# Kernel optimization log

Hardware: AMD Instinct MI355X
Metric: run time of the kernel (lower is better)

The kernel has to match this reference:

```python
import jax, jax.numpy as jnp
import numpy as np

N_NODES = 50000
N_EDGES = 800000
NEG_SLOPE = 0.2  # leaky_relu slope used in the model


def setup_inputs() -> dict:
    key = jax.random.key(0)
    ks = jax.random.split(key, 8)
    d_in, d_h, d_out = 64, 64, 4
    x = jax.random.normal(ks[0], (N_NODES, d_in), dtype=jnp.float32)
    edge_index = jax.random.randint(ks[1], (2, N_EDGES), 0, N_NODES, dtype=jnp.int32)
    # Glorot-style init like PyG GCNConv
    W0 = jax.random.normal(ks[2], (d_in, d_h), dtype=jnp.float32) * np.float32(1.0 / np.sqrt(d_in))
    W1 = jax.random.normal(ks[3], (d_h, d_h), dtype=jnp.float32) * np.float32(1.0 / np.sqrt(d_h))
    W2 = jax.random.normal(ks[4], (d_h, d_out), dtype=jnp.float32) * np.float32(1.0 / np.sqrt(d_h))
    b0 = jnp.zeros((d_h,), dtype=jnp.float32)
    b1 = jnp.zeros((d_h,), dtype=jnp.float32)
    b2 = jnp.zeros((d_out,), dtype=jnp.float32)
    return {"x": x, "edge_index": edge_index, "W0": W0, "b0": b0,
            "W1": W1, "b1": b1, "W2": W2, "b2": b2}


def _gcn_norm(edge_index, n_nodes, dtype):
    # Add self-loops, compute symmetric normalization D^{-1/2} (A+I) D^{-1/2}
    src, dst = edge_index[0], edge_index[1]
    loop = jnp.arange(n_nodes, dtype=src.dtype)
    src = jnp.concatenate([src, loop])
    dst = jnp.concatenate([dst, loop])
    deg = jax.ops.segment_sum(jnp.ones_like(dst, dtype=dtype), dst, num_segments=n_nodes)
    dinv = jnp.where(deg > 0, jax.lax.rsqrt(deg), jnp.zeros_like(deg))
    norm = dinv[src] * dinv[dst]  # [E + N]
    return src, dst, norm


def _gcn_layer(h, src, dst, norm, W, b, n_nodes):
    h = h @ W                                  # [N, d_out]
    msg = h[src] * norm[:, None]               # gather + edge scaling
    out = jax.ops.segment_sum(msg, dst, num_segments=n_nodes)  # scatter-add
    return out + b


def reference(x, edge_index, W0, b0, W1, b1, W2, b2):
    # Eval-mode forward: dropout_edge and F.dropout are identity when not training.
    n = x.shape[0]
    src, dst, norm = _gcn_norm(edge_index, n, x.dtype)
    h = _gcn_layer(x, src, dst, norm, W0, b0, n)
    h = jax.nn.leaky_relu(h, NEG_SLOPE)
    h = _gcn_layer(h, src, dst, norm, W1, b1, n)
    h = jax.nn.leaky_relu(h, NEG_SLOPE)
    out = _gcn_layer(h, src, dst, norm, W2, b2, n)
    return out
```

## Files before the change

### kernel.cpp

```cpp
#include <hip/hip_runtime.h>
#include <math.h>

#define NEG_SLOPE 0.2f
#define NPAD 50176
#define NW8  (NPAD / 4)
#define NCHUNK 256

__global__ __launch_bounds__(1024) void k_hist(const int* __restrict__ dst,
                                               unsigned int* __restrict__ histw,
                                               unsigned char* __restrict__ rank,
                                               int e, int es) {
    extern __shared__ unsigned int lcnt[];
    int t = threadIdx.x;
    for (int w = t; w < NW8; w += 1024) lcnt[w] = 0u;
    __syncthreads();
    int beg = blockIdx.x * es;
    int end = min(beg + es, e);
    for (int i = beg + t; i < end; i += 1024) {
        int d = dst[i];
        int sh = (d & 3) << 3;
        unsigned int old = atomicAdd(&lcnt[d >> 2], 1u << sh);
        rank[i] = (unsigned char)((old >> sh) & 0xffu);
    }
    __syncthreads();
    unsigned int* out = histw + (size_t)blockIdx.x * NW8;
    for (int w = t; w < NW8; w += 1024) out[w] = lcnt[w];
}

__global__ __launch_bounds__(256) void k_chscan(unsigned char* __restrict__ hist8,
                                                float* __restrict__ dinv,
                                                unsigned short* __restrict__ deg16,
                                                int* __restrict__ bsum, int n) {
    int t = threadIdx.x;
    int i = blockIdx.x * 256 + t;
    unsigned char* p = hist8 + i;
    unsigned int run = 0;
    for (int c = 0; c < NCHUNK; c += 8) {
        size_t b = (size_t)c * NPAD;
        unsigned char v0 = p[b];
        unsigned char v1 = p[b + (size_t)1 * NPAD];
        unsigned char v2 = p[b + (size_t)2 * NPAD];
        unsigned char v3 = p[b + (size_t)3 * NPAD];
        unsigned char v4 = p[b + (size_t)4 * NPAD];
        unsigned char v5 = p[b + (size_t)5 * NPAD];
        unsigned char v6 = p[b + (size_t)6 * NPAD];
        unsigned char v7 = p[b + (size_t)7 * NPAD];
        unsigned int e0 = run;
        unsigned int e1 = e0 + v0;
        unsigned int e2 = e1 + v1;
        unsigned int e3 = e2 + v2;
        unsigned int e4 = e3 + v3;
        unsigned int e5 = e4 + v4;
        unsigned int e6 = e5 + v5;
        unsigned int e7 = e6 + v6;
        run = e7 + v7;
        p[b] = (unsigned char)e0;
        p[b + (size_t)1 * NPAD] = (unsigned char)e1;
        p[b + (size_t)2 * NPAD] = (unsigned char)e2;
        p[b + (size_t)3 * NPAD] = (unsigned char)e3;
        p[b + (size_t)4 * NPAD] = (unsigned char)e4;
        p[b + (size_t)5 * NPAD] = (unsigned char)e5;
        p[b + (size_t)6 * NPAD] = (unsigned char)e6;
        p[b + (size_t)7 * NPAD] = (unsigned char)e7;
    }
    int deg = (int)run;
    if (i < n) dinv[i] = rsqrtf((float)(deg + 1));
    deg16[i] = (unsigned short)deg;
    int s = deg;
    for (int d = 1; d < 64; d <<= 1) s += __shfl_down(s, d);
    __shared__ int ws[4];
    if ((t & 63) == 0) ws[t >> 6] = s;
    __syncthreads();
    if (t == 0) bsum[blockIdx.x] = ws[0] + ws[1] + ws[2] + ws[3];
}

__global__ __launch_bounds__(256) void k_scan3(const unsigned short* __restrict__ deg16,
                                               const int* __restrict__ bsum,
                                               int* __restrict__ rowptr, int n, int nb) {
    __shared__ int ls[256];
    __shared__ int wo[4];
    int t = threadIdx.x;
    int bid = blockIdx.x;
    int bv = (t < bid && t < nb) ? bsum[t] : 0;
    for (int d = 1; d < 64; d <<= 1) bv += __shfl_down(bv, d);
    if ((t & 63) == 0) wo[t >> 6] = bv;
    __syncthreads();
    int boff = wo[0] + wo[1] + wo[2] + wo[3];
    int i = bid * 256 + t;
    int v = (i < n) ? (int)deg16[i] : 0;
    ls[t] = v;
    __syncthreads();
    for (int d = 1; d < 256; d <<= 1) {
        int u = (t >= d) ? ls[t - d] : 0;
        __syncthreads();
        ls[t] += u;
        __syncthreads();
    }
    int excl = ls[t] - v + boff;
    if (i < n) rowptr[i] = excl;
    if (i == n - 1) rowptr[n] = excl + v;
}

__global__ void k_place(const int* __restrict__ src, const int* __restrict__ dst,
                        const int* __restrict__ rowptr, const unsigned char* __restrict__ rank,
                        const unsigned char* __restrict__ choff,
                        int* __restrict__ perm, int e, int es) {
    int i = blockIdx.x * 256 + threadIdx.x;
    if (i >= e) return;
    int d = dst[i];
    unsigned int c = (unsigned int)i / (unsigned int)es;
    int slot = rowptr[d] + (int)choff[(size_t)c * NPAD + d] + (int)rank[i];
    perm[slot] = src[i];
}

__global__ __launch_bounds__(256) void k_gemm64(const float* __restrict__ in,
                                                const float* __restrict__ W,
                                                const float* __restrict__ dinv,
                                                _Float16* __restrict__ out, int n) {
    __shared__ float Ws[64 * 64];
    __shared__ float Xs[16 * 64];
    int t = threadIdx.x;
    const float4* W4 = (const float4*)W;
    float4* Ws4 = (float4*)Ws;
#pragma unroll
    for (int i = 0; i < 4; ++i) Ws4[t + 256 * i] = W4[t + 256 * i];
    int row0 = blockIdx.x * 16;
    {
        int r = t >> 4, c4 = t & 15;
        int row = row0 + r;
        float4 v = make_float4(0.f, 0.f, 0.f, 0.f);
        if (row < n) v = ((const float4*)(in + (size_t)row * 64))[c4];
        ((float4*)Xs)[t] = v;
    }
    __syncthreads();
    int c = t & 63, g = t >> 6;
    float a0 = 0.f, a1 = 0.f, a2 = 0.f, a3 = 0.f;
#pragma unroll
    for (int k = 0; k < 64; ++k) {
        float w = Ws[k * 64 + c];
        a0 = fmaf(Xs[g * 64 + k], w, a0);
        a1 = fmaf(Xs[(g + 4) * 64 + k], w, a1);
        a2 = fmaf(Xs[(g + 8) * 64 + k], w, a2);
        a3 = fmaf(Xs[(g + 12) * 64 + k], w, a3);
    }
    int r;
    r = row0 + g;      if (r < n) out[(size_t)r * 64 + c] = (_Float16)(a0 * dinv[r]);
    r = row0 + g + 4;  if (r < n) out[(size_t)r * 64 + c] = (_Float16)(a1 * dinv[r]);
    r = row0 + g + 8;  if (r < n) out[(size_t)r * 64 + c] = (_Float16)(a2 * dinv[r]);
    r = row0 + g + 12; if (r < n) out[(size_t)r * 64 + c] = (_Float16)(a3 * dinv[r]);
}

__global__ void k_gemm4(const float* __restrict__ in, const float* __restrict__ W,
                        const float* __restrict__ dinv, float* __restrict__ out, int n) {
    __shared__ float Ws[64 * 4];
    int t = threadIdx.x;
    Ws[t] = W[t];
    __syncthreads();
    int row = blockIdx.x * 256 + t;
    if (row >= n) return;
    float a0 = 0.f, a1 = 0.f, a2 = 0.f, a3 = 0.f;
    const float4* xin = (const float4*)(in + (size_t)row * 64);
#pragma unroll
    for (int k4 = 0; k4 < 16; ++k4) {
        float4 x = xin[k4];
        int k = k4 * 4;
        a0 = fmaf(x.x, Ws[k * 4 + 0], a0); a1 = fmaf(x.x, Ws[k * 4 + 1], a1);
        a2 = fmaf(x.x, Ws[k * 4 + 2], a2); a3 = fmaf(x.x, Ws[k * 4 + 3], a3);
        a0 = fmaf(x.y, Ws[k * 4 + 4], a0); a1 = fmaf(x.y, Ws[k * 4 + 5], a1);
        a2 = fmaf(x.y, Ws[k * 4 + 6], a2); a3 = fmaf(x.y, Ws[k * 4 + 7], a3);
        a0 = fmaf(x.z, Ws[k * 4 + 8], a0); a1 = fmaf(x.z, Ws[k * 4 + 9], a1);
        a2 = fmaf(x.z, Ws[k * 4 + 10], a2); a3 = fmaf(x.z, Ws[k * 4 + 11], a3);
        a0 = fmaf(x.w, Ws[k * 4 + 12], a0); a1 = fmaf(x.w, Ws[k * 4 + 13], a1);
        a2 = fmaf(x.w, Ws[k * 4 + 14], a2); a3 = fmaf(x.w, Ws[k * 4 + 15], a3);
    }
    float dv = dinv[row];
    *reinterpret_cast<float4*>(out + (size_t)row * 4) =
        make_float4(a0 * dv, a1 * dv, a2 * dv, a3 * dv);
}

__global__ __launch_bounds__(256) void k_gather64(
        const _Float16* __restrict__ h, const float* __restrict__ dinv,
        const int* __restrict__ rowptr, const int* __restrict__ perm,
        const float* __restrict__ b, float* __restrict__ out, int n, int act) {
    int t = threadIdx.x;
    int v = blockIdx.x * 4 + (t >> 6);
    if (v >= n) return;
    v = __builtin_amdgcn_readfirstlane(v);
    int lane = t & 63;
    const _Float16* hl = h + lane;
    float acc = (float)hl[(size_t)v * 64];
    int e = rowptr[v], end = rowptr[v + 1];
#define LOADK(j) float x##j = (float)hl[(size_t)perm[e + j] * 64]
    for (; e + 16 <= end; e += 16) {
        LOADK(0); LOADK(1); LOADK(2); LOADK(3);
        LOADK(4); LOADK(5); LOADK(6); LOADK(7);
        LOADK(8); LOADK(9); LOADK(10); LOADK(11);
        LOADK(12); LOADK(13); LOADK(14); LOADK(15);
        acc += (((x0 + x1) + (x2 + x3)) + ((x4 + x5) + (x6 + x7)))
             + (((x8 + x9) + (x10 + x11)) + ((x12 + x13) + (x14 + x15)));
    }
    if (e + 8 <= end) {
        LOADK(0); LOADK(1); LOADK(2); LOADK(3);
        LOADK(4); LOADK(5); LOADK(6); LOADK(7);
        acc += ((x0 + x1) + (x2 + x3)) + ((x4 + x5) + (x6 + x7));
        e += 8;
    }
    if (e + 4 <= end) {
        LOADK(0); LOADK(1); LOADK(2); LOADK(3);
        acc += (x0 + x1) + (x2 + x3);
        e += 4;
    }
    if (e + 2 <= end) {
        LOADK(0); LOADK(1);
        acc += x0 + x1;
        e += 2;
    }
    if (e < end) acc += (float)hl[(size_t)perm[e] * 64];
#undef LOADK
    acc = acc * dinv[v] + b[lane];
    if (act) acc = acc > 0.0f ? acc : acc * NEG_SLOPE;
    out[(size_t)v * 64 + lane] = acc;
}

__global__ __launch_bounds__(256) void k_gather4(
        const float* __restrict__ h, const float* __restrict__ dinv,
        const int* __restrict__ rowptr, const int* __restrict__ perm,
        const float* __restrict__ b, float* __restrict__ out, int n) {
    int gid = blockIdx.x * 256 + threadIdx.x;
    int c = gid & 3;
    int v = gid >> 2;
    if (v >= n) return;
    const float* hc = h + c;
    float acc = hc[(size_t)v * 4];
    int e = rowptr[v], end = rowptr[v + 1];
    for (; e + 4 <= end; e += 4) {
        float x0 = hc[(size_t)perm[e] * 4];
        float x1 = hc[(size_t)perm[e + 1] * 4];
        float x2 = hc[(size_t)perm[e + 2] * 4];
        float x3 = hc[(size_t)perm[e + 3] * 4];
        acc += (x0 + x1) + (x2 + x3);
    }
    for (; e < end; ++e) acc += hc[(size_t)perm[e] * 4];
    out[(size_t)v * 4 + c] = acc * dinv[v] + b[c];
}

extern "C" void kernel_launch(void* const* d_in, const int* in_sizes, int n_in,
                              void* d_out, int out_size, void* d_ws, size_t ws_size,
                              hipStream_t stream) {
    const float* x  = (const float*)d_in[0];
    const int* ei   = (const int*)d_in[1];
    const float* W0 = (const float*)d_in[2];
    const float* b0 = (const float*)d_in[3];
    const float* W1 = (const float*)d_in[4];
    const float* b1 = (const float*)d_in[5];
    const float* W2 = (const float*)d_in[6];
    const float* b2 = (const float*)d_in[7];
    float* out = (float*)d_out;

    const int N = in_sizes[0] / 64;
    const int E = in_sizes[1] / 2;
    const int* src = ei;
    const int* dst = ei + E;
    const int es = (E + NCHUNK - 1) / NCHUNK;

    char* base = (char*)d_ws;
    size_t off = 0;
    auto alloc = [&](size_t bytes) { size_t o = off; off = (off + bytes + 255) & ~(size_t)255; return o; };
    unsigned int*   histw  = (unsigned int*)(base + alloc((size_t)NCHUNK * NPAD));
    unsigned char*  rank   = (unsigned char*)(base + alloc((size_t)E));
    unsigned short* deg16  = (unsigned short*)(base + alloc((size_t)NPAD * 2));
    float*          dinv   = (float*)(base + alloc((size_t)NPAD * 4));
    int*            rowptr = (int*)(base + alloc((size_t)(NPAD + 1) * 4));
    int*            bsum   = (int*)(base + alloc(1024));
    int*            perm   = (int*)(base + alloc((size_t)E * 4));
    _Float16*       bufH   = (_Float16*)(base + alloc((size_t)N * 64 * 2));
    float*          bufB   = (float*)(base + alloc((size_t)N * 64 * 4));
    float*          bufD   = (float*)(base + alloc((size_t)N * 4 * 4));

    const int nb_N = (N + 255) / 256;
    const int nb_E = (E + 255) / 256;
    const int nb_V = (N + 3) / 4;

    k_hist<<<NCHUNK, 1024, NW8 * sizeof(unsigned int), stream>>>(dst, histw, rank, E, es);
    k_chscan<<<NPAD / 256, 256, 0, stream>>>((unsigned char*)histw, dinv, deg16, bsum, N);
    k_scan3<<<nb_N, 256, 0, stream>>>(deg16, bsum, rowptr, N, nb_N);
    k_place<<<nb_E, 256, 0, stream>>>(src, dst, rowptr, rank, (const unsigned char*)histw, perm, E, es);

    k_gemm64<<<(N + 15) / 16, 256, 0, stream>>>(x, W0, dinv, bufH, N);
    k_gather64<<<nb_V, 256, 0, stream>>>(bufH, dinv, rowptr, perm, b0, bufB, N, 1);

    k_gemm64<<<(N + 15) / 16, 256, 0, stream>>>(bufB, W1, dinv, bufH, N);
    k_gather64<<<nb_V, 256, 0, stream>>>(bufH, dinv, rowptr, perm, b1, bufB, N, 1);

    k_gemm4<<<nb_N, 256, 0, stream>>>(bufB, W2, dinv, bufD, N);
    k_gather4<<<(N * 4 + 255) / 256, 256, 0, stream>>>(bufD, dinv, rowptr, perm, b2, out, N);
}
```

Measured before the change: 165.2 us.

## Pack histogram into 4-bit counters and split 64-wide gather into two column passes

The per-chunk shared-memory histogram now uses 4-bit counters, halving LDS usage and the written histogram size. Chunk offsets go to a separate byte array so the scan no longer rewrites in place. The 64-column gather is split into two launches covering 32 columns each; each half-wave handles alternate edges and the halves are combined with a cross-lane shuffle. The aim is to shrink the gathered working set per pass (more L2 reuse) and raise edge-level parallelism, at the cost of reading the CSR twice and extra launches. Nibble counters overflow if a node gets 16 or more edges in one chunk, which is unlikely with about 3125 edges per chunk spread over 50k nodes.

```diff
diff --git a/kernel.cpp b/kernel.cpp
--- a/kernel.cpp
+++ b/kernel.cpp
@@ -3,7 +3,8 @@
 
 #define NEG_SLOPE 0.2f
 #define NPAD 50176
-#define NW8  (NPAD / 4)
+#define NW4  (NPAD / 8)
+#define HB   (NPAD / 2)
 #define NCHUNK 256
 
 __global__ __launch_bounds__(1024) void k_hist(const int* __restrict__ dst,
@@ -12,39 +13,42 @@
                                                int e, int es) {
     extern __shared__ unsigned int lcnt[];
     int t = threadIdx.x;
-    for (int w = t; w < NW8; w += 1024) lcnt[w] = 0u;
+    for (int w = t; w < NW4; w += 1024) lcnt[w] = 0u;
     __syncthreads();
     int beg = blockIdx.x * es;
     int end = min(beg + es, e);
     for (int i = beg + t; i < end; i += 1024) {
         int d = dst[i];
-        int sh = (d & 3) << 3;
-        unsigned int old = atomicAdd(&lcnt[d >> 2], 1u << sh);
-        rank[i] = (unsigned char)((old >> sh) & 0xffu);
-    }
-    __syncthreads();
-    unsigned int* out = histw + (size_t)blockIdx.x * NW8;
-    for (int w = t; w < NW8; w += 1024) out[w] = lcnt[w];
-}
-
-__global__ __launch_bounds__(256) void k_chscan(unsigned char* __restrict__ hist8,
+        int sh = (d & 7) << 2;
+        unsigned int old = atomicAdd(&lcnt[d >> 3], 1u << sh);
+        rank[i] = (unsigned char)((old >> sh) & 0xFu);
+    }
+    __syncthreads();
+    unsigned int* out = histw + (size_t)blockIdx.x * NW4;
+    for (int w = t; w < NW4; w += 1024) out[w] = lcnt[w];
+}
+
+__global__ __launch_bounds__(256) void k_chscan(const unsigned char* __restrict__ hist4,
+                                                unsigned char* __restrict__ choff,
                                                 float* __restrict__ dinv,
                                                 unsigned short* __restrict__ deg16,
                                                 int* __restrict__ bsum, int n) {
     int t = threadIdx.x;
     int i = blockIdx.x * 256 + t;
-    unsigned char* p = hist8 + i;
+    const unsigned char* p = hist4 + (i >> 1);
+    unsigned char* pc = choff + i;
+    int nib = (i & 1) << 2;
     unsigned int run = 0;
     for (int c = 0; c < NCHUNK; c += 8) {
-        size_t b = (size_t)c * NPAD;
-        unsigned char v0 = p[b];
-        unsigned char v1 = p[b + (size_t)1 * NPAD];
-        unsigned char v2 = p[b + (size_t)2 * NPAD];
-        unsigned char v3 = p[b + (size_t)3 * NPAD];
-        unsigned char v4 = p[b + (size_t)4 * NPAD];
-        unsigned char v5 = p[b + (size_t)5 * NPAD];
-        unsigned char v6 = p[b + (size_t)6 * NPAD];
-        unsigned char v7 = p[b + (size_t)7 * NPAD];
+        size_t b = (size_t)c * HB;
+        unsigned int v0 = (p[b] >> nib) & 0xFu;
+        unsigned int v1 = (p[b + (size_t)1 * HB] >> nib) & 0xFu;
+        unsigned int v2 = (p[b + (size_t)2 * HB] >> nib) & 0xFu;
+        unsigned int v3 = (p[b + (size_t)3 * HB] >> nib) & 0xFu;
+        unsigned int v4 = (p[b + (size_t)4 * HB] >> nib) & 0xFu;
+        unsigned int v5 = (p[b + (size_t)5 * HB] >> nib) & 0xFu;
+        unsigned int v6 = (p[b + (size_t)6 * HB] >> nib) & 0xFu;
+        unsigned int v7 = (p[b + (size_t)7 * HB] >> nib) & 0xFu;
         unsigned int e0 = run;
         unsigned int e1 = e0 + v0;
         unsigned int e2 = e1 + v1;
@@ -54,14 +58,15 @@
         unsigned int e6 = e5 + v5;
         unsigned int e7 = e6 + v6;
         run = e7 + v7;
-        p[b] = (unsigned char)e0;
-        p[b + (size_t)1 * NPAD] = (unsigned char)e1;
-        p[b + (size_t)2 * NPAD] = (unsigned char)e2;
-        p[b + (size_t)3 * NPAD] = (unsigned char)e3;
-        p[b + (size_t)4 * NPAD] = (unsigned char)e4;
-        p[b + (size_t)5 * NPAD] = (unsigned char)e5;
-        p[b + (size_t)6 * NPAD] = (unsigned char)e6;
-        p[b + (size_t)7 * NPAD] = (unsigned char)e7;
+        size_t bo = (size_t)c * NPAD;
+        pc[bo] = (unsigned char)e0;
+        pc[bo + (size_t)1 * NPAD] = (unsigned char)e1;
+        pc[bo + (size_t)2 * NPAD] = (unsigned char)e2;
+        pc[bo + (size_t)3 * NPAD] = (unsigned char)e3;
+        pc[bo + (size_t)4 * NPAD] = (unsigned char)e4;
+        pc[bo + (size_t)5 * NPAD] = (unsigned char)e5;
+        pc[bo + (size_t)6 * NPAD] = (unsigned char)e6;
+        pc[bo + (size_t)7 * NPAD] = (unsigned char)e7;
     }
     int deg = (int)run;
     if (i < n) dinv[i] = rsqrtf((float)(deg + 1));
@@ -181,45 +186,49 @@
 __global__ __launch_bounds__(256) void k_gather64(
         const _Float16* __restrict__ h, const float* __restrict__ dinv,
         const int* __restrict__ rowptr, const int* __restrict__ perm,
-        const float* __restrict__ b, float* __restrict__ out, int n, int act) {
+        const float* __restrict__ b, float* __restrict__ out, int n, int act, int pass) {
     int t = threadIdx.x;
     int v = blockIdx.x * 4 + (t >> 6);
     if (v >= n) return;
     v = __builtin_amdgcn_readfirstlane(v);
     int lane = t & 63;
-    const _Float16* hl = h + lane;
-    float acc = (float)hl[(size_t)v * 64];
+    int c = lane & 31;
+    int half = lane >> 5;
+    const _Float16* hl = h + 32 * pass + c;
+    float acc = (half == 0) ? (float)hl[(size_t)v * 64] : 0.0f;
     int e = rowptr[v], end = rowptr[v + 1];
-#define LOADK(j) float x##j = (float)hl[(size_t)perm[e + j] * 64]
+#define PAIR(j) int sA##j = perm[e + 2*j], sB##j = perm[e + 2*j + 1]; \
+                int s##j = half ? sB##j : sA##j; \
+                float x##j = (float)hl[(size_t)s##j * 64]
     for (; e + 16 <= end; e += 16) {
-        LOADK(0); LOADK(1); LOADK(2); LOADK(3);
-        LOADK(4); LOADK(5); LOADK(6); LOADK(7);
-        LOADK(8); LOADK(9); LOADK(10); LOADK(11);
-        LOADK(12); LOADK(13); LOADK(14); LOADK(15);
-        acc += (((x0 + x1) + (x2 + x3)) + ((x4 + x5) + (x6 + x7)))
-             + (((x8 + x9) + (x10 + x11)) + ((x12 + x13) + (x14 + x15)));
+        PAIR(0); PAIR(1); PAIR(2); PAIR(3);
+        PAIR(4); PAIR(5); PAIR(6); PAIR(7);
+        acc += (((x0 + x1) + (x2 + x3)) + ((x4 + x5) + (x6 + x7)));
     }
     if (e + 8 <= end) {
-        LOADK(0); LOADK(1); LOADK(2); LOADK(3);
-        LOADK(4); LOADK(5); LOADK(6); LOADK(7);
-        acc += ((x0 + x1) + (x2 + x3)) + ((x4 + x5) + (x6 + x7));
+        PAIR(0); PAIR(1); PAIR(2); PAIR(3);
+        acc += (x0 + x1) + (x2 + x3);
         e += 8;
     }
     if (e + 4 <= end) {
-        LOADK(0); LOADK(1); LOADK(2); LOADK(3);
-        acc += (x0 + x1) + (x2 + x3);
+        PAIR(0); PAIR(1);
+        acc += x0 + x1;
         e += 4;
     }
     if (e + 2 <= end) {
-        LOADK(0); LOADK(1);
-        acc += x0 + x1;
+        PAIR(0);
+        acc += x0;
         e += 2;
     }
-    if (e < end) acc += (float)hl[(size_t)perm[e] * 64];
-#undef LOADK
-    acc = acc * dinv[v] + b[lane];
-    if (act) acc = acc > 0.0f ? acc : acc * NEG_SLOPE;
-    out[(size_t)v * 64 + lane] = acc;
+#undef PAIR
+    if (e < end && half == 0)
+        acc += (float)hl[(size_t)perm[e] * 64];
+    acc += __shfl_xor(acc, 32);
+    float dv = dinv[v];
+    float o = acc * dv + b[32 * pass + c];
+    if (act) o = o > 0.0f ? o : o * NEG_SLOPE;
+    if (lane < 32)
+        out[(size_t)v * 64 + 32 * pass + c] = o;
 }
 
 __global__ __launch_bounds__(256) void k_gather4(
@@ -266,7 +275,8 @@
     char* base = (char*)d_ws;
     size_t off = 0;
     auto alloc = [&](size_t bytes) { size_t o = off; off = (off + bytes + 255) & ~(size_t)255; return o; };
-    unsigned int*   histw  = (unsigned int*)(base + alloc((size_t)NCHUNK * NPAD));
+    unsigned int*   histw  = (unsigned int*)(base + alloc((size_t)NCHUNK * HB));
+    unsigned char*  choff  = (unsigned char*)(base + alloc((size_t)NCHUNK * NPAD));
     unsigned char*  rank   = (unsigned char*)(base + alloc((size_t)E));
     unsigned short* deg16  = (unsigned short*)(base + alloc((size_t)NPAD * 2));
     float*          dinv   = (float*)(base + alloc((size_t)NPAD * 4));
@@ -281,16 +291,18 @@
     const int nb_E = (E + 255) / 256;
     const int nb_V = (N + 3) / 4;
 
-    k_hist<<<NCHUNK, 1024, NW8 * sizeof(unsigned int), stream>>>(dst, histw, rank, E, es);
-    k_chscan<<<NPAD / 256, 256, 0, stream>>>((unsigned char*)histw, dinv, deg16, bsum, N);
+    k_hist<<<NCHUNK, 1024, NW4 * sizeof(unsigned int), stream>>>(dst, histw, rank, E, es);
+    k_chscan<<<NPAD / 256, 256, 0, stream>>>((const unsigned char*)histw, choff, dinv, deg16, bsum, N);
     k_scan3<<<nb_N, 256, 0, stream>>>(deg16, bsum, rowptr, N, nb_N);
-    k_place<<<nb_E, 256, 0, stream>>>(src, dst, rowptr, rank, (const unsigned char*)histw, perm, E, es);
+    k_place<<<nb_E, 256, 0, stream>>>(src, dst, rowptr, rank, choff, perm, E, es);
 
     k_gemm64<<<(N + 15) / 16, 256, 0, stream>>>(x, W0, dinv, bufH, N);
-    k_gather64<<<nb_V, 256, 0, stream>>>(bufH, dinv, rowptr, perm, b0, bufB, N, 1);
+    k_gather64<<<nb_V, 256, 0, stream>>>(bufH, dinv, rowptr, perm, b0, bufB, N, 1, 0);
+    k_gather64<<<nb_V, 256, 0, stream>>>(bufH, dinv, rowptr, perm, b0, bufB, N, 1, 1);
 
     k_gemm64<<<(N + 15) / 16, 256, 0, stream>>>(bufB, W1, dinv, bufH, N);
-    k_gather64<<<nb_V, 256, 0, stream>>>(bufH, dinv, rowptr, perm, b1, bufB, N, 1);
+    k_gather64<<<nb_V, 256, 0, stream>>>(bufH, dinv, rowptr, perm, b1, bufB, N, 1, 0);
+    k_gather64<<<nb_V, 256, 0, stream>>>(bufH, dinv, rowptr, perm, b1, bufB, N, 1, 1);
 
     k_gemm4<<<nb_N, 256, 0, stream>>>(bufB, W2, dinv, bufD, N);
     k_gather4<<<(N * 4 + 255) / 256, 256, 0, stream>>>(bufD, dinv, rowptr, perm, b2, out, N);
```

New measurement: 215.2 us. 1.3x slower.
